# Optimization experiments

Hardware: AMD Instinct MI355X
Metric: run time of the kernel (lower is better)

## Reference

```python
import jax, jax.numpy as jnp
import numpy as np
from jax.scipy.linalg import expm

N, D, COND_DIM = 1152, 64, 1152
B, T = 16, 1024


def setup_inputs() -> dict:
    key = jax.random.key(0)
    k1, k2, k3, k4, k5 = jax.random.split(key, 5)
    x = jax.random.normal(k1, (B, T, N), dtype=jnp.float32)
    cond = jax.random.normal(k2, (B, COND_DIM), dtype=jnp.float32)
    # learned parameters
    P = jax.random.normal(k3, (N, D), dtype=jnp.float32)
    n_skew = D * (D - 1) // 2
    # nn.Linear default init: U(-1/sqrt(fan_in), 1/sqrt(fan_in))
    bound = 1.0 / np.sqrt(COND_DIM)
    W = jax.random.uniform(k4, (n_skew, COND_DIM), minval=-bound, maxval=bound, dtype=jnp.float32)
    b = jax.random.uniform(k5, (n_skew,), minval=-bound, maxval=bound, dtype=jnp.float32)
    return {"x": x, "cond": cond, "P": P, "W": W, "b": b}


def _rotation(cond, W, b):
    # SiLU -> Linear -> skew-symmetric A -> matrix exponential
    v = jax.nn.silu(cond) @ W.T + b  # (B, D*(D-1)//2)
    iu, ju = jnp.triu_indices(D, k=1)
    A = jnp.zeros((cond.shape[0], D, D), dtype=v.dtype)
    A = A.at[:, iu, ju].set(v).at[:, ju, iu].set(-v)
    return expm(A)  # batched over leading dim, (B, D, D)


def reference(x, cond, P, W, b):
    U, _ = jnp.linalg.qr(P)          # (N, D) orthonormal basis of subspace
    R = _rotation(cond, W, b)        # (B, D, D)
    z = jnp.einsum('btn,nd->btd', x, U)          # project into subspace
    z_rot = jnp.einsum('btd,bde->bte', z, R)     # rotate within subspace
    x_rot = x + jnp.einsum('btd,nd->btn', z_rot - z, U)  # (z_rot - z) @ U.T
    return x_rot
```

## Files before the change

kernel.cpp:

```cpp
#include <hip/hip_runtime.h>
#include <math.h>

#define NN 1152
#define DD 64
#define NSK 2016
#define NB 16
#define NROWS (NB*1024)
#define GPARTS 6

typedef short bf16x8 __attribute__((ext_vector_type(8)));
typedef float f32x4  __attribute__((ext_vector_type(4)));

__device__ __forceinline__ short bfr(float f){
  unsigned u = __float_as_uint(f);
  u += 0x7fffu + ((u >> 16) & 1u);
  return (short)(u >> 16);
}

__global__ __launch_bounds__(256) void k_pre(const float* __restrict__ cond, const float* __restrict__ W,
                                             const float* __restrict__ bias, float* __restrict__ v,
                                             const float* __restrict__ P, float* __restrict__ Gpart){
  __shared__ float Ps[64*68];
  __shared__ float red[256*17];
  const int tid = threadIdx.x;
  if (blockIdx.x < NSK){
    const int q = blockIdx.x;
    float acc[NB];
    #pragma unroll
    for (int b = 0; b < NB; ++b) acc[b] = 0.f;
    for (int c = tid; c < NN; c += 256){
      const float wv = W[q*NN + c];
      #pragma unroll
      for (int b = 0; b < NB; ++b){
        const float xv = cond[b*NN + c];
        const float s = xv / (1.f + __expf(-xv));
        acc[b] = fmaf(wv, s, acc[b]);
      }
    }
    #pragma unroll
    for (int b = 0; b < NB; ++b) red[tid*17 + b] = acc[b];
    __syncthreads();
    for (int off = 128; off > 0; off >>= 1){
      if (tid < off){
        #pragma unroll
        for (int b = 0; b < NB; ++b) red[tid*17 + b] += red[(tid+off)*17 + b];
      }
      __syncthreads();
    }
    if (tid < NB) v[tid*NSK + q] = red[tid] + bias[q];
  } else {
    const int p = blockIdx.x - NSK;
    const int lr = tid >> 4, lc = (tid & 15) * 4;
    const int ti = tid >> 4, tj = tid & 15;
    float acc[4][4];
    #pragma unroll
    for (int i=0;i<4;++i){
      #pragma unroll
      for (int j=0;j<4;++j) acc[i][j]=0.f;
    }
    for (int ch = 0; ch < 3; ++ch){
      const int n0 = p*192 + ch*64;
      __syncthreads();
      #pragma unroll
      for (int ii = 0; ii < 4; ++ii){
        const float4 pv = *(const float4*)&P[(n0 + lr + 16*ii)*DD + lc];
        *(float4*)&Ps[(lr + 16*ii)*68 + lc] = pv;
      }
      __syncthreads();
      for (int r = 0; r < 64; ++r){
        const float4 a = *(const float4*)&Ps[r*68 + ti*4];
        const float4 b = *(const float4*)&Ps[r*68 + tj*4];
        const float av[4] = {a.x,a.y,a.z,a.w};
        const float bv[4] = {b.x,b.y,b.z,b.w};
        #pragma unroll
        for (int i=0;i<4;++i){
          #pragma unroll
          for (int j=0;j<4;++j) acc[i][j] = fmaf(av[i], bv[j], acc[i][j]);
        }
      }
    }
    float* g = &Gpart[p*DD*DD];
    #pragma unroll
    for (int i=0;i<4;++i){
      float4 ov = make_float4(acc[i][0], acc[i][1], acc[i][2], acc[i][3]);
      *(float4*)&g[(ti*4+i)*DD + tj*4] = ov;
    }
  }
}

__device__ void qr_wave(const float* __restrict__ Gpart, const float* __restrict__ P,
                        float* __restrict__ Rout){
  const int j = threadIdx.x;
  float Gc[DD], Wc[DD], Rc[DD];
  #pragma unroll
  for (int i = 0; i < DD; ++i){
    float g = 0.f;
    #pragma unroll
    for (int p = 0; p < GPARTS; ++p) g += Gpart[p*4096 + i*DD + j];
    Gc[i] = g;
    Wc[i] = P[i*DD + j];
  }
  #pragma unroll
  for (int k = 0; k < DD; ++k){
    const float gkk = __shfl(Gc[k], k);
    const float wkk = __shfl(Wc[k], k);
    const float beta = (wkk >= 0.f) ? -sqrtf(gkk) : sqrtf(gkk);
    const float wkj = Wc[k];
    const float dj  = Gc[k] - beta*wkj;
    const float cj  = dj / (beta*(beta - wkk));
    float rkj = wkj + dj/beta;
    if (j == k) rkj = beta;
    if (j <  k) rkj = 0.f;
    Rc[k] = rkj;
    #pragma unroll
    for (int i = k+1; i < DD; ++i){
      const float wik = __shfl(Wc[i], k);
      const float rki = __shfl(rkj, i);
      Wc[i] = fmaf(-cj,  wik, Wc[i]);
      Gc[i] = fmaf(-rki, rkj, Gc[i]);
    }
  }
  #pragma unroll
  for (int i = 0; i < DD; ++i) Rout[i*DD + j] = Rc[i];
}

__device__ __forceinline__ void mmul68(const float* __restrict__ A, const float* __restrict__ B,
                                       float* __restrict__ C, int tid){
  __syncthreads();
  const int ty = tid >> 4, tx = tid & 15;
  float acc[4][4];
  #pragma unroll
  for (int i=0;i<4;++i){
    #pragma unroll
    for (int j=0;j<4;++j) acc[i][j]=0.f;
  }
  for (int kq = 0; kq < 16; ++kq){
    float4 a[4], b[4];
    #pragma unroll
    for (int i=0;i<4;++i) a[i] = *(const float4*)&A[(ty*4+i)*68 + kq*4];
    #pragma unroll
    for (int kk=0;kk<4;++kk) b[kk] = *(const float4*)&B[(kq*4+kk)*68 + tx*4];
    #pragma unroll
    for (int i=0;i<4;++i){
      const float av[4] = {a[i].x, a[i].y, a[i].z, a[i].w};
      #pragma unroll
      for (int kk=0;kk<4;++kk){
        acc[i][0] = fmaf(av[kk], b[kk].x, acc[i][0]);
        acc[i][1] = fmaf(av[kk], b[kk].y, acc[i][1]);
        acc[i][2] = fmaf(av[kk], b[kk].z, acc[i][2]);
        acc[i][3] = fmaf(av[kk], b[kk].w, acc[i][3]);
      }
    }
  }
  #pragma unroll
  for (int i=0;i<4;++i)
    *(float4*)&C[(ty*4+i)*68 + tx*4] = make_float4(acc[i][0],acc[i][1],acc[i][2],acc[i][3]);
  __syncthreads();
}

__global__ __launch_bounds__(256,1) void k_setup(const float* __restrict__ Gpart, const float* __restrict__ P,
                                                 float* __restrict__ Rout,
                                                 const float* __restrict__ v, float* __restrict__ Mg){
  __shared__ float Bs[64*68], B2[64*68], B3[64*68], Tb[64*68], Xb[64*68];
  __shared__ float ncol[DD];
  __shared__ float scl_s;
  __shared__ int   ssh_s;
  const int tid = threadIdx.x;
  if (blockIdx.x == NB){
    if (tid >= 64) return;
    qr_wave(Gpart, P, Rout);
    return;
  }
  const int b = blockIdx.x;
  for (int idx = tid; idx < 64*64; idx += 256)
    Xb[(idx>>6)*68 + (idx&63)] = 0.f;
  __syncthreads();
  for (int idx = tid; idx < NSK; idx += 256){
    int i = (int)((127.0f - sqrtf(16129.0f - 8.0f*(float)idx)) * 0.5f);
    while (i*(127 - i)/2 > idx) --i;
    while ((i+1)*(127 - (i+1))/2 <= idx) ++i;
    const int jj = idx - i*(127 - i)/2 + i + 1;
    const float val = v[b*NSK + idx];
    Xb[i*68 + jj] = val;
    Xb[jj*68 + i] = -val;
  }
  __syncthreads();
  if (tid < DD){
    float s = 0.f;
    for (int r = 0; r < DD; ++r) s += fabsf(Xb[r*68 + tid]);
    ncol[tid] = s;
  }
  __syncthreads();
  if (tid == 0){
    float nrm = 0.f;
    for (int c = 0; c < DD; ++c) nrm = fmaxf(nrm, ncol[c]);
    int s = 0; float scale = 1.f;
    while (nrm > 1.0f && s < 40){ nrm *= 0.5f; scale *= 0.5f; ++s; }
    ssh_s = s; scl_s = scale;
  }
  __syncthreads();
  const float scale = scl_s;
  const int   sq    = ssh_s;
  for (int idx = tid; idx < 64*64; idx += 256){
    const int i = idx>>6, jj = idx&63;
    Bs[i*68 + jj] = Xb[i*68 + jj] * scale;
  }
  mmul68(Bs, Bs, B2, tid);
  mmul68(B2, Bs, B3, tid);
  for (int idx = tid; idx < 64*64; idx += 256){
    const int i = idx>>6, jj = idx&63;
    const int o = i*68 + jj;
    Tb[o] = (i==jj ? (1.f/720.f) : 0.f) + Bs[o]*(1.f/5040.f) + B2[o]*(1.f/40320.f) + B3[o]*(1.f/362880.f);
  }
  mmul68(B3, Tb, Xb, tid);
  for (int idx = tid; idx < 64*64; idx += 256){
    const int i = idx>>6, jj = idx&63;
    const int o = i*68 + jj;
    Xb[o] += (i==jj ? (1.f/6.f) : 0.f) + Bs[o]*(1.f/24.f) + B2[o]*(1.f/120.f);
  }
  mmul68(B3, Xb, Tb, tid);
  for (int idx = tid; idx < 64*64; idx += 256){
    const int i = idx>>6, jj = idx&63;
    const int o = i*68 + jj;
    Tb[o] += (i==jj ? 1.f : 0.f) + Bs[o] + B2[o]*0.5f;
  }
  float* cur = Tb;
  float* oth = Xb;
  for (int r = 0; r < sq; ++r){
    mmul68(cur, cur, oth, tid);
    float* t = cur; cur = oth; oth = t;
  }
  for (int idx = tid; idx < 64*64; idx += 256){
    const int i = idx>>6, jj = idx&63;
    Mg[b*4096 + idx] = cur[i*68 + jj] - (i==jj ? 1.f : 0.f);
  }
}

__global__ __launch_bounds__(64) void k_solveU(const float* __restrict__ P, const float* __restrict__ Rg,
                                               short* __restrict__ Ubf, short* __restrict__ Utbf){
  __shared__ float Rs[DD*DD];
  __shared__ float Ps[DD*65];
  __shared__ float rd[DD];
  const int tid = threadIdx.x;
  const int n0 = blockIdx.x * DD;
  for (int r = 0; r < DD; ++r){
    Rs[r*DD + tid] = Rg[r*DD + tid];
    Ps[r*65 + tid] = P[(n0 + r)*DD + tid];
  }
  rd[tid] = 1.f / Rg[tid*DD + tid];
  __syncthreads();
  float u[DD];
  #pragma unroll
  for (int j = 0; j < DD; ++j){
    float s0 = Ps[tid*65 + j], s1 = 0.f;
    #pragma unroll
    for (int l = 0; l + 1 < j; l += 2){
      s0 = fmaf(-u[l],   Rs[l*DD + j],     s0);
      s1 = fmaf(-u[l+1], Rs[(l+1)*DD + j], s1);
    }
    if (j & 1) s0 = fmaf(-u[j-1], Rs[(j-1)*DD + j], s0);
    u[j] = (s0 + s1) * rd[j];
  }
  #pragma unroll
  for (int d = 0; d < DD; ++d)
    Utbf[d*NN + n0 + tid] = bfr(u[d]);
  #pragma unroll
  for (int j8 = 0; j8 < 8; ++j8){
    bf16x8 pk;
    #pragma unroll
    for (int jj = 0; jj < 8; ++jj) pk[jj] = bfr(u[j8*8 + jj]);
    *(bf16x8*)&Ubf[(n0 + tid)*DD + j8*8] = pk;
  }
}

__global__ __launch_bounds__(512,1) void k_main(const float* __restrict__ x, const short* __restrict__ Ubf,
                                                const short* __restrict__ Utbf, const float* __restrict__ Mg,
                                                float* __restrict__ out){
  __shared__ float zs[64*68];
  __shared__ float Ms[64*68];
  __shared__ short wbf[64*72];
  const int tid  = threadIdx.x;
  const int lane = tid & 63, wid = tid >> 6;
  const int row0 = blockIdx.x * 64;
  const int bb   = row0 >> 10;
  const int m    = lane & 15, quad = lane >> 4;
  for (int idx = tid; idx < 64*64; idx += 512)
    Ms[(idx>>6)*68 + (idx&63)] = Mg[bb*4096 + idx];

  const int r0 = (wid & 3) * 16;
  const int c0 = (wid >> 2) * 32;
  f32x4 acc0 = {0.f,0.f,0.f,0.f}, acc1 = {0.f,0.f,0.f,0.f};
  const float* xrow = &x[(row0 + r0 + m)*NN + quad*8];
  const short* ut0  = &Utbf[(c0      + m)*NN + quad*8];
  const short* ut1  = &Utbf[(c0 + 16 + m)*NN + quad*8];
  float4 xa = *(const float4*)(xrow);
  float4 xb = *(const float4*)(xrow + 4);
  bf16x8 b0 = *(const bf16x8*)(ut0);
  bf16x8 b1 = *(const bf16x8*)(ut1);
  for (int kc = 0; kc < NN; kc += 32){
    float4 nxa, nxb; bf16x8 nb0, nb1;
    if (kc + 32 < NN){
      nxa = *(const float4*)(xrow + kc + 32);
      nxb = *(const float4*)(xrow + kc + 36);
      nb0 = *(const bf16x8*)(ut0 + kc + 32);
      nb1 = *(const bf16x8*)(ut1 + kc + 32);
    }
    bf16x8 a;
    a[0]=bfr(xa.x); a[1]=bfr(xa.y); a[2]=bfr(xa.z); a[3]=bfr(xa.w);
    a[4]=bfr(xb.x); a[5]=bfr(xb.y); a[6]=bfr(xb.z); a[7]=bfr(xb.w);
    acc0 = __builtin_amdgcn_mfma_f32_16x16x32_bf16(a, b0, acc0, 0, 0, 0);
    acc1 = __builtin_amdgcn_mfma_f32_16x16x32_bf16(a, b1, acc1, 0, 0, 0);
    xa = nxa; xb = nxb; b0 = nb0; b1 = nb1;
  }
  #pragma unroll
  for (int q = 0; q < 4; ++q){
    zs[(r0 + quad*4 + q)*68 + c0      + m] = acc0[q];
    zs[(r0 + quad*4 + q)*68 + c0 + 16 + m] = acc1[q];
  }
  __syncthreads();

  {
    const int r  = tid >> 3;
    const int cc = (tid & 7) * 8;
    float w0[8];
    #pragma unroll
    for (int jj = 0; jj < 8; ++jj) w0[jj] = 0.f;
    for (int k = 0; k < 64; ++k){
      const float zr = zs[r*68 + k];
      const float4 m0 = *(const float4*)&Ms[k*68 + cc];
      const float4 m1 = *(const float4*)&Ms[k*68 + cc + 4];
      w0[0] = fmaf(zr, m0.x, w0[0]); w0[1] = fmaf(zr, m0.y, w0[1]);
      w0[2] = fmaf(zr, m0.z, w0[2]); w0[3] = fmaf(zr, m0.w, w0[3]);
      w0[4] = fmaf(zr, m1.x, w0[4]); w0[5] = fmaf(zr, m1.y, w0[5]);
      w0[6] = fmaf(zr, m1.z, w0[6]); w0[7] = fmaf(zr, m1.w, w0[7]);
    }
    bf16x8 pk;
    #pragma unroll
    for (int jj = 0; jj < 8; ++jj) pk[jj] = bfr(w0[jj]);
    *(bf16x8*)&wbf[r*72 + cc] = pk;
  }
  __syncthreads();

  bf16x8 wa0 = *(const bf16x8*)&wbf[(r0 + m)*72 +      quad*8];
  bf16x8 wa1 = *(const bf16x8*)&wbf[(r0 + m)*72 + 32 + quad*8];
  const int colpar = wid >> 2;
  for (int it = 0; it < 36; ++it){
    const int n0 = (colpar + 2*it) * 16;
    bf16x8 ub0 = *(const bf16x8*)&Ubf[(n0 + m)*DD +      quad*8];
    bf16x8 ub1 = *(const bf16x8*)&Ubf[(n0 + m)*DD + 32 + quad*8];
    f32x4 acc = {0.f,0.f,0.f,0.f};
    acc = __builtin_amdgcn_mfma_f32_16x16x32_bf16(wa0, ub0, acc, 0, 0, 0);
    acc = __builtin_amdgcn_mfma_f32_16x16x32_bf16(wa1, ub1, acc, 0, 0, 0);
    #pragma unroll
    for (int q = 0; q < 4; ++q){
      const int r = row0 + r0 + quad*4 + q;
      const int c = n0 + m;
      out[r*NN + c] = x[r*NN + c] + acc[q];
    }
  }
}

extern "C" void kernel_launch(void* const* d_in, const int* in_sizes, int n_in,
                              void* d_out, int out_size, void* d_ws, size_t ws_size,
                              hipStream_t stream) {
  const float* x    = (const float*)d_in[0];
  const float* cond = (const float*)d_in[1];
  const float* P    = (const float*)d_in[2];
  const float* W    = (const float*)d_in[3];
  const float* bias = (const float*)d_in[4];
  float* out = (float*)d_out;
  float* ws  = (float*)d_ws;

  float* Gpart = ws;
  float* Rbuf  = ws + 24576;
  float* vbuf  = ws + 28672;
  float* Mg    = ws + 61440;
  short* Ubf   = (short*)(ws + 126976);
  short* Utbf  = (short*)(ws + 163840);

  hipLaunchKernelGGL(k_pre,   dim3(NSK + GPARTS), dim3(256), 0, stream, cond, W, bias, vbuf, P, Gpart);
  hipLaunchKernelGGL(k_setup, dim3(NB + 1),       dim3(256), 0, stream, Gpart, P, Rbuf, vbuf, Mg);
  hipLaunchKernelGGL(k_solveU,dim3(NN/DD),        dim3(64),  0, stream, P, Rbuf, Ubf, Utbf);
  hipLaunchKernelGGL(k_main,  dim3(NROWS/64),     dim3(512), 0, stream, x, Ubf, Utbf, Mg, out);
}
```

Before: 285.2 us.

## Shrink main-kernel row tiles for occupancy and restructure conditioning GEMV

The main kernel now handles 16 rows per 256-thread block instead of 64 rows per 512-thread block, with launch bounds allowing 4 blocks per CU, and double-buffers x/U loads with a 64-wide k step. Its output phase prefetches the next U tile. The SiLU+linear prologue now computes SiLU once per block into shared memory, assigns one wave per output row using float4 loads, and reduces with wave shuffles instead of a shared-memory tree. The aim is more latency hiding and less redundant SiLU work, at the cost of loading the 64x64 M matrix four times as often and reading each U tile from more blocks.

Result: slower. 319.5 us (+12.0%).

```diff
diff --git a/kernel.cpp b/kernel.cpp
--- a/kernel.cpp
+++ b/kernel.cpp
@@ -7,8 +7,11 @@
 #define NB 16
 #define NROWS (NB*1024)
 #define GPARTS 6
+#define QPB 4
+#define VPB (NSK/QPB)
 
 typedef short bf16x8 __attribute__((ext_vector_type(8)));
+typedef short bf16x4 __attribute__((ext_vector_type(4)));
 typedef float f32x4  __attribute__((ext_vector_type(4)));
 
 __device__ __forceinline__ short bfr(float f){
@@ -20,36 +23,49 @@
 __global__ __launch_bounds__(256) void k_pre(const float* __restrict__ cond, const float* __restrict__ W,
                                              const float* __restrict__ bias, float* __restrict__ v,
                                              const float* __restrict__ P, float* __restrict__ Gpart){
-  __shared__ float Ps[64*68];
-  __shared__ float red[256*17];
+  __shared__ float smem[16*1160];
   const int tid = threadIdx.x;
-  if (blockIdx.x < NSK){
-    const int q = blockIdx.x;
+  if (blockIdx.x < VPB){
+    #pragma unroll
+    for (int b = 0; b < NB; ++b){
+      for (int c = tid; c < NN; c += 256){
+        const float xv = cond[b*NN + c];
+        smem[b*1160 + c] = xv / (1.f + __expf(-xv));
+      }
+    }
+    __syncthreads();
+    const int lane = tid & 63, wid = tid >> 6;
+    const int q = blockIdx.x * QPB + wid;
     float acc[NB];
     #pragma unroll
     for (int b = 0; b < NB; ++b) acc[b] = 0.f;
-    for (int c = tid; c < NN; c += 256){
-      const float wv = W[q*NN + c];
+    for (int c0 = 0; c0 < NN; c0 += 256){
+      const int c = c0 + lane*4;
+      if (c < NN){
+        const float4 wv = *(const float4*)&W[q*NN + c];
+        #pragma unroll
+        for (int b = 0; b < NB; ++b){
+          const float4 sv = *(const float4*)&smem[b*1160 + c];
+          acc[b] = fmaf(wv.x, sv.x, acc[b]);
+          acc[b] = fmaf(wv.y, sv.y, acc[b]);
+          acc[b] = fmaf(wv.z, sv.z, acc[b]);
+          acc[b] = fmaf(wv.w, sv.w, acc[b]);
+        }
+      }
+    }
+    #pragma unroll
+    for (int off = 32; off > 0; off >>= 1){
       #pragma unroll
-      for (int b = 0; b < NB; ++b){
-        const float xv = cond[b*NN + c];
-        const float s = xv / (1.f + __expf(-xv));
-        acc[b] = fmaf(wv, s, acc[b]);
-      }
-    }
-    #pragma unroll
-    for (int b = 0; b < NB; ++b) red[tid*17 + b] = acc[b];
-    __syncthreads();
-    for (int off = 128; off > 0; off >>= 1){
-      if (tid < off){
-        #pragma unroll
-        for (int b = 0; b < NB; ++b) red[tid*17 + b] += red[(tid+off)*17 + b];
-      }
-      __syncthreads();
-    }
-    if (tid < NB) v[tid*NSK + q] = red[tid] + bias[q];
+      for (int b = 0; b < NB; ++b) acc[b] += __shfl_xor(acc[b], off);
+    }
+    if (lane == 0){
+      const float bq = bias[q];
+      #pragma unroll
+      for (int b = 0; b < NB; ++b) v[b*NSK + q] = acc[b] + bq;
+    }
   } else {
-    const int p = blockIdx.x - NSK;
+    float* Ps = smem;
+    const int p = blockIdx.x - VPB;
     const int lr = tid >> 4, lc = (tid & 15) * 4;
     const int ti = tid >> 4, tj = tid & 15;
     float acc[4][4];
@@ -273,91 +289,102 @@
   }
 }
 
-__global__ __launch_bounds__(512,1) void k_main(const float* __restrict__ x, const short* __restrict__ Ubf,
+#define PH1_STEP(XA,XB,UU) do { \
+    bf16x8 a_; \
+    a_[0]=bfr(XA.x); a_[1]=bfr(XA.y); a_[2]=bfr(XA.z); a_[3]=bfr(XA.w); \
+    a_[4]=bfr(XB.x); a_[5]=bfr(XB.y); a_[6]=bfr(XB.z); a_[7]=bfr(XB.w); \
+    acc0 = __builtin_amdgcn_mfma_f32_16x16x32_bf16(a_, UU, acc0, 0, 0, 0); \
+  } while(0)
+
+#define PH3_BODY(NC) do { \
+    const float xq0 = x[(row0 + quad*4 + 0)*NN + (NC) + m]; \
+    const float xq1 = x[(row0 + quad*4 + 1)*NN + (NC) + m]; \
+    const float xq2 = x[(row0 + quad*4 + 2)*NN + (NC) + m]; \
+    const float xq3 = x[(row0 + quad*4 + 3)*NN + (NC) + m]; \
+    f32x4 acc = {0.f,0.f,0.f,0.f}; \
+    acc = __builtin_amdgcn_mfma_f32_16x16x32_bf16(wa0, ub0, acc, 0, 0, 0); \
+    acc = __builtin_amdgcn_mfma_f32_16x16x32_bf16(wa1, ub1, acc, 0, 0, 0); \
+    out[(row0 + quad*4 + 0)*NN + (NC) + m] = xq0 + acc[0]; \
+    out[(row0 + quad*4 + 1)*NN + (NC) + m] = xq1 + acc[1]; \
+    out[(row0 + quad*4 + 2)*NN + (NC) + m] = xq2 + acc[2]; \
+    out[(row0 + quad*4 + 3)*NN + (NC) + m] = xq3 + acc[3]; \
+  } while(0)
+
+__global__ __launch_bounds__(256,4) void k_main(const float* __restrict__ x, const short* __restrict__ Ubf,
                                                 const short* __restrict__ Utbf, const float* __restrict__ Mg,
                                                 float* __restrict__ out){
-  __shared__ float zs[64*68];
   __shared__ float Ms[64*68];
-  __shared__ short wbf[64*72];
+  __shared__ float zs[16*68];
+  __shared__ short wbf[16*72];
   const int tid  = threadIdx.x;
   const int lane = tid & 63, wid = tid >> 6;
-  const int row0 = blockIdx.x * 64;
+  const int row0 = blockIdx.x * 16;
   const int bb   = row0 >> 10;
   const int m    = lane & 15, quad = lane >> 4;
-  for (int idx = tid; idx < 64*64; idx += 512)
+  for (int idx = tid; idx < 64*64; idx += 256)
     Ms[(idx>>6)*68 + (idx&63)] = Mg[bb*4096 + idx];
 
-  const int r0 = (wid & 3) * 16;
-  const int c0 = (wid >> 2) * 32;
-  f32x4 acc0 = {0.f,0.f,0.f,0.f}, acc1 = {0.f,0.f,0.f,0.f};
-  const float* xrow = &x[(row0 + r0 + m)*NN + quad*8];
-  const short* ut0  = &Utbf[(c0      + m)*NN + quad*8];
-  const short* ut1  = &Utbf[(c0 + 16 + m)*NN + quad*8];
-  float4 xa = *(const float4*)(xrow);
-  float4 xb = *(const float4*)(xrow + 4);
-  bf16x8 b0 = *(const bf16x8*)(ut0);
-  bf16x8 b1 = *(const bf16x8*)(ut1);
-  for (int kc = 0; kc < NN; kc += 32){
-    float4 nxa, nxb; bf16x8 nb0, nb1;
-    if (kc + 32 < NN){
-      nxa = *(const float4*)(xrow + kc + 32);
-      nxb = *(const float4*)(xrow + kc + 36);
-      nb0 = *(const bf16x8*)(ut0 + kc + 32);
-      nb1 = *(const bf16x8*)(ut1 + kc + 32);
-    }
-    bf16x8 a;
-    a[0]=bfr(xa.x); a[1]=bfr(xa.y); a[2]=bfr(xa.z); a[3]=bfr(xa.w);
-    a[4]=bfr(xb.x); a[5]=bfr(xb.y); a[6]=bfr(xb.z); a[7]=bfr(xb.w);
-    acc0 = __builtin_amdgcn_mfma_f32_16x16x32_bf16(a, b0, acc0, 0, 0, 0);
-    acc1 = __builtin_amdgcn_mfma_f32_16x16x32_bf16(a, b1, acc1, 0, 0, 0);
-    xa = nxa; xb = nxb; b0 = nb0; b1 = nb1;
-  }
-  #pragma unroll
-  for (int q = 0; q < 4; ++q){
-    zs[(r0 + quad*4 + q)*68 + c0      + m] = acc0[q];
-    zs[(r0 + quad*4 + q)*68 + c0 + 16 + m] = acc1[q];
-  }
+  const int c0 = wid * 16;
+  const float* xrow = &x[(row0 + m)*NN + quad*8];
+  const short* utp  = &Utbf[(c0 + m)*NN + quad*8];
+  f32x4 acc0 = {0.f,0.f,0.f,0.f};
+  float4 xa0 = *(const float4*)(xrow);
+  float4 xb0 = *(const float4*)(xrow + 4);
+  float4 xa1 = *(const float4*)(xrow + 32);
+  float4 xb1 = *(const float4*)(xrow + 36);
+  bf16x8 u0  = *(const bf16x8*)(utp);
+  bf16x8 u1  = *(const bf16x8*)(utp + 32);
+  for (int kc = 0; kc < NN - 64; kc += 64){
+    const float4 pxa0 = *(const float4*)(xrow + kc + 64);
+    const float4 pxb0 = *(const float4*)(xrow + kc + 68);
+    const bf16x8 pu0  = *(const bf16x8*)(utp + kc + 64);
+    const float4 pxa1 = *(const float4*)(xrow + kc + 96);
+    const float4 pxb1 = *(const float4*)(xrow + kc + 100);
+    const bf16x8 pu1  = *(const bf16x8*)(utp + kc + 96);
+    PH1_STEP(xa0, xb0, u0);
+    PH1_STEP(xa1, xb1, u1);
+    xa0 = pxa0; xb0 = pxb0; u0 = pu0;
+    xa1 = pxa1; xb1 = pxb1; u1 = pu1;
+  }
+  PH1_STEP(xa0, xb0, u0);
+  PH1_STEP(xa1, xb1, u1);
+  #pragma unroll
+  for (int q = 0; q < 4; ++q)
+    zs[(quad*4 + q)*68 + c0 + m] = acc0[q];
   __syncthreads();
 
   {
-    const int r  = tid >> 3;
-    const int cc = (tid & 7) * 8;
-    float w0[8];
-    #pragma unroll
-    for (int jj = 0; jj < 8; ++jj) w0[jj] = 0.f;
+    const int r  = tid >> 4;
+    const int cc = (tid & 15) * 4;
+    float w0[4] = {0.f,0.f,0.f,0.f};
     for (int k = 0; k < 64; ++k){
       const float zr = zs[r*68 + k];
       const float4 m0 = *(const float4*)&Ms[k*68 + cc];
-      const float4 m1 = *(const float4*)&Ms[k*68 + cc + 4];
-      w0[0] = fmaf(zr, m0.x, w0[0]); w0[1] = fmaf(zr, m0.y, w0[1]);
-      w0[2] = fmaf(zr, m0.z, w0[2]); w0[3] = fmaf(zr, m0.w, w0[3]);
-      w0[4] = fmaf(zr, m1.x, w0[4]); w0[5] = fmaf(zr, m1.y, w0[5]);
-      w0[6] = fmaf(zr, m1.z, w0[6]); w0[7] = fmaf(zr, m1.w, w0[7]);
-    }
-    bf16x8 pk;
-    #pragma unroll
-    for (int jj = 0; jj < 8; ++jj) pk[jj] = bfr(w0[jj]);
-    *(bf16x8*)&wbf[r*72 + cc] = pk;
-  }
-  __syncthreads();
-
-  bf16x8 wa0 = *(const bf16x8*)&wbf[(r0 + m)*72 +      quad*8];
-  bf16x8 wa1 = *(const bf16x8*)&wbf[(r0 + m)*72 + 32 + quad*8];
-  const int colpar = wid >> 2;
-  for (int it = 0; it < 36; ++it){
-    const int n0 = (colpar + 2*it) * 16;
-    bf16x8 ub0 = *(const bf16x8*)&Ubf[(n0 + m)*DD +      quad*8];
-    bf16x8 ub1 = *(const bf16x8*)&Ubf[(n0 + m)*DD + 32 + quad*8];
-    f32x4 acc = {0.f,0.f,0.f,0.f};
-    acc = __builtin_amdgcn_mfma_f32_16x16x32_bf16(wa0, ub0, acc, 0, 0, 0);
-    acc = __builtin_amdgcn_mfma_f32_16x16x32_bf16(wa1, ub1, acc, 0, 0, 0);
-    #pragma unroll
-    for (int q = 0; q < 4; ++q){
-      const int r = row0 + r0 + quad*4 + q;
-      const int c = n0 + m;
-      out[r*NN + c] = x[r*NN + c] + acc[q];
-    }
-  }
+      w0[0] = fmaf(zr, m0.x, w0[0]);
+      w0[1] = fmaf(zr, m0.y, w0[1]);
+      w0[2] = fmaf(zr, m0.z, w0[2]);
+      w0[3] = fmaf(zr, m0.w, w0[3]);
+    }
+    bf16x4 pk;
+    #pragma unroll
+    for (int jj = 0; jj < 4; ++jj) pk[jj] = bfr(w0[jj]);
+    *(bf16x4*)&wbf[r*72 + cc] = pk;
+  }
+  __syncthreads();
+
+  bf16x8 wa0 = *(const bf16x8*)&wbf[m*72 +      quad*8];
+  bf16x8 wa1 = *(const bf16x8*)&wbf[m*72 + 32 + quad*8];
+  bf16x8 ub0 = *(const bf16x8*)&Ubf[(wid*16 + m)*DD +      quad*8];
+  bf16x8 ub1 = *(const bf16x8*)&Ubf[(wid*16 + m)*DD + 32 + quad*8];
+  for (int it = 0; it < 17; ++it){
+    const int n0c = (wid + 4*it) * 16;
+    const int n1  = n0c + 64;
+    const bf16x8 nb0 = *(const bf16x8*)&Ubf[(n1 + m)*DD +      quad*8];
+    const bf16x8 nb1 = *(const bf16x8*)&Ubf[(n1 + m)*DD + 32 + quad*8];
+    PH3_BODY(n0c);
+    ub0 = nb0; ub1 = nb1;
+  }
+  PH3_BODY((wid + 68) * 16);
 }
 
 extern "C" void kernel_launch(void* const* d_in, const int* in_sizes, int n_in,
@@ -378,8 +405,8 @@
   short* Ubf   = (short*)(ws + 126976);
   short* Utbf  = (short*)(ws + 163840);
 
-  hipLaunchKernelGGL(k_pre,   dim3(NSK + GPARTS), dim3(256), 0, stream, cond, W, bias, vbuf, P, Gpart);
+  hipLaunchKernelGGL(k_pre,   dim3(VPB + GPARTS), dim3(256), 0, stream, cond, W, bias, vbuf, P, Gpart);
   hipLaunchKernelGGL(k_setup, dim3(NB + 1),       dim3(256), 0, stream, Gpart, P, Rbuf, vbuf, Mg);
   hipLaunchKernelGGL(k_solveU,dim3(NN/DD),        dim3(64),  0, stream, P, Rbuf, Ubf, Utbf);
-  hipLaunchKernelGGL(k_main,  dim3(NROWS/64),     dim3(512), 0, stream, x, Ubf, Utbf, Mg, out);
-}
+  hipLaunchKernelGGL(k_main,  dim3(NROWS/16),     dim3(256), 0, stream, x, Ubf, Utbf, Mg, out);
+}
```

## Use MFMA split-K for cond linear and split main kernel into zw and output passes

Applied to the files above, without the earlier changes.

The SiLU-linear producing the skew parameters now runs as bf16 MFMA tiles split over six K partitions. The partial sums are reduced, with the bias added, inside the setup kernel. This replaces the per-output-row block with its shared-memory tree reduction. The main kernel is also split in two: one computes the rotated projection w and writes it to global memory as bf16, and a new lighter output kernel with many more blocks does the U^T expansion plus residual with prefetched loads. The split is meant to raise occupancy and parallelism for the store-bound phase, at the cost of an extra kernel launch, a second read of x, and bf16 rounding of cond and W.

After: 265.7 us. -6.8%, faster.

```diff
diff --git a/kernel.cpp b/kernel.cpp
--- a/kernel.cpp
+++ b/kernel.cpp
@@ -7,8 +7,12 @@
 #define NB 16
 #define NROWS (NB*1024)
 #define GPARTS 6
+#define KPARTS 6
+#define VNBLK 32
+#define VBLKS (VNBLK*KPARTS)
 
 typedef short bf16x8 __attribute__((ext_vector_type(8)));
+typedef short bf16x4 __attribute__((ext_vector_type(4)));
 typedef float f32x4  __attribute__((ext_vector_type(4)));
 
 __device__ __forceinline__ short bfr(float f){
@@ -18,38 +22,42 @@
 }
 
 __global__ __launch_bounds__(256) void k_pre(const float* __restrict__ cond, const float* __restrict__ W,
-                                             const float* __restrict__ bias, float* __restrict__ v,
+                                             float* __restrict__ vpart,
                                              const float* __restrict__ P, float* __restrict__ Gpart){
   __shared__ float Ps[64*68];
-  __shared__ float red[256*17];
   const int tid = threadIdx.x;
-  if (blockIdx.x < NSK){
-    const int q = blockIdx.x;
-    float acc[NB];
-    #pragma unroll
-    for (int b = 0; b < NB; ++b) acc[b] = 0.f;
-    for (int c = tid; c < NN; c += 256){
-      const float wv = W[q*NN + c];
+  if (blockIdx.x < VBLKS){
+    const int nb = blockIdx.x / KPARTS;
+    const int kp = blockIdx.x % KPARTS;
+    const int lane = tid & 63, wid = tid >> 6;
+    const int m = lane & 15, quad = lane >> 4;
+    const int n0 = nb*64 + wid*16;
+    if (n0 >= NSK) return;
+    f32x4 acc = {0.f,0.f,0.f,0.f};
+    const float* crow = &cond[m*NN + kp*192 + quad*8];
+    const float* wrow = &W[(n0 + m)*NN + kp*192 + quad*8];
+    #pragma unroll
+    for (int c = 0; c < 6; ++c){
+      const float4 ca = *(const float4*)(crow + c*32);
+      const float4 cb = *(const float4*)(crow + c*32 + 4);
+      const float4 wa = *(const float4*)(wrow + c*32);
+      const float4 wb = *(const float4*)(wrow + c*32 + 4);
+      bf16x8 a, b;
+      const float cv[8] = {ca.x,ca.y,ca.z,ca.w,cb.x,cb.y,cb.z,cb.w};
+      const float wv[8] = {wa.x,wa.y,wa.z,wa.w,wb.x,wb.y,wb.z,wb.w};
       #pragma unroll
-      for (int b = 0; b < NB; ++b){
-        const float xv = cond[b*NN + c];
-        const float s = xv / (1.f + __expf(-xv));
-        acc[b] = fmaf(wv, s, acc[b]);
+      for (int j = 0; j < 8; ++j){
+        const float xv = cv[j];
+        a[j] = bfr(xv / (1.f + __expf(-xv)));
+        b[j] = bfr(wv[j]);
       }
-    }
-    #pragma unroll
-    for (int b = 0; b < NB; ++b) red[tid*17 + b] = acc[b];
-    __syncthreads();
-    for (int off = 128; off > 0; off >>= 1){
-      if (tid < off){
-        #pragma unroll
-        for (int b = 0; b < NB; ++b) red[tid*17 + b] += red[(tid+off)*17 + b];
-      }
-      __syncthreads();
-    }
-    if (tid < NB) v[tid*NSK + q] = red[tid] + bias[q];
+      acc = __builtin_amdgcn_mfma_f32_16x16x32_bf16(a, b, acc, 0, 0, 0);
+    }
+    #pragma unroll
+    for (int r = 0; r < 4; ++r)
+      vpart[(kp*16 + quad*4 + r)*NSK + n0 + m] = acc[r];
   } else {
-    const int p = blockIdx.x - NSK;
+    const int p = blockIdx.x - VBLKS;
     const int lr = tid >> 4, lc = (tid & 15) * 4;
     const int ti = tid >> 4, tj = tid & 15;
     float acc[4][4];
@@ -59,11 +67,11 @@
       for (int j=0;j<4;++j) acc[i][j]=0.f;
     }
     for (int ch = 0; ch < 3; ++ch){
-      const int n0 = p*192 + ch*64;
+      const int nn0 = p*192 + ch*64;
       __syncthreads();
       #pragma unroll
       for (int ii = 0; ii < 4; ++ii){
-        const float4 pv = *(const float4*)&P[(n0 + lr + 16*ii)*DD + lc];
+        const float4 pv = *(const float4*)&P[(nn0 + lr + 16*ii)*DD + lc];
         *(float4*)&Ps[(lr + 16*ii)*68 + lc] = pv;
       }
       __syncthreads();
@@ -160,7 +168,8 @@
 
 __global__ __launch_bounds__(256,1) void k_setup(const float* __restrict__ Gpart, const float* __restrict__ P,
                                                  float* __restrict__ Rout,
-                                                 const float* __restrict__ v, float* __restrict__ Mg){
+                                                 const float* __restrict__ vpart, const float* __restrict__ bias,
+                                                 float* __restrict__ Mg){
   __shared__ float Bs[64*68], B2[64*68], B3[64*68], Tb[64*68], Xb[64*68];
   __shared__ float ncol[DD];
   __shared__ float scl_s;
@@ -180,7 +189,9 @@
     while (i*(127 - i)/2 > idx) --i;
     while ((i+1)*(127 - (i+1))/2 <= idx) ++i;
     const int jj = idx - i*(127 - i)/2 + i + 1;
-    const float val = v[b*NSK + idx];
+    float val = bias[idx];
+    #pragma unroll
+    for (int p = 0; p < KPARTS; ++p) val += vpart[(p*16 + b)*NSK + idx];
     Xb[i*68 + jj] = val;
     Xb[jj*68 + i] = -val;
   }
@@ -273,12 +284,10 @@
   }
 }
 
-__global__ __launch_bounds__(512,1) void k_main(const float* __restrict__ x, const short* __restrict__ Ubf,
-                                                const short* __restrict__ Utbf, const float* __restrict__ Mg,
-                                                float* __restrict__ out){
+__global__ __launch_bounds__(512,1) void k_zw(const float* __restrict__ x, const short* __restrict__ Utbf,
+                                              const float* __restrict__ Mg, short* __restrict__ wg){
   __shared__ float zs[64*68];
   __shared__ float Ms[64*68];
-  __shared__ short wbf[64*72];
   const int tid  = threadIdx.x;
   const int lane = tid & 63, wid = tid >> 6;
   const int row0 = blockIdx.x * 64;
@@ -319,44 +328,63 @@
   }
   __syncthreads();
 
-  {
-    const int r  = tid >> 3;
-    const int cc = (tid & 7) * 8;
-    float w0[8];
-    #pragma unroll
-    for (int jj = 0; jj < 8; ++jj) w0[jj] = 0.f;
-    for (int k = 0; k < 64; ++k){
-      const float zr = zs[r*68 + k];
-      const float4 m0 = *(const float4*)&Ms[k*68 + cc];
-      const float4 m1 = *(const float4*)&Ms[k*68 + cc + 4];
-      w0[0] = fmaf(zr, m0.x, w0[0]); w0[1] = fmaf(zr, m0.y, w0[1]);
-      w0[2] = fmaf(zr, m0.z, w0[2]); w0[3] = fmaf(zr, m0.w, w0[3]);
-      w0[4] = fmaf(zr, m1.x, w0[4]); w0[5] = fmaf(zr, m1.y, w0[5]);
-      w0[6] = fmaf(zr, m1.z, w0[6]); w0[7] = fmaf(zr, m1.w, w0[7]);
-    }
-    bf16x8 pk;
-    #pragma unroll
-    for (int jj = 0; jj < 8; ++jj) pk[jj] = bfr(w0[jj]);
-    *(bf16x8*)&wbf[r*72 + cc] = pk;
-  }
-  __syncthreads();
-
-  bf16x8 wa0 = *(const bf16x8*)&wbf[(r0 + m)*72 +      quad*8];
-  bf16x8 wa1 = *(const bf16x8*)&wbf[(r0 + m)*72 + 32 + quad*8];
-  const int colpar = wid >> 2;
-  for (int it = 0; it < 36; ++it){
-    const int n0 = (colpar + 2*it) * 16;
-    bf16x8 ub0 = *(const bf16x8*)&Ubf[(n0 + m)*DD +      quad*8];
-    bf16x8 ub1 = *(const bf16x8*)&Ubf[(n0 + m)*DD + 32 + quad*8];
+  const int r  = tid >> 3;
+  const int cc = (tid & 7) * 8;
+  float w0[8];
+  #pragma unroll
+  for (int jj = 0; jj < 8; ++jj) w0[jj] = 0.f;
+  for (int k = 0; k < 64; ++k){
+    const float zr = zs[r*68 + k];
+    const float4 m0 = *(const float4*)&Ms[k*68 + cc];
+    const float4 m1 = *(const float4*)&Ms[k*68 + cc + 4];
+    w0[0] = fmaf(zr, m0.x, w0[0]); w0[1] = fmaf(zr, m0.y, w0[1]);
+    w0[2] = fmaf(zr, m0.z, w0[2]); w0[3] = fmaf(zr, m0.w, w0[3]);
+    w0[4] = fmaf(zr, m1.x, w0[4]); w0[5] = fmaf(zr, m1.y, w0[5]);
+    w0[6] = fmaf(zr, m1.z, w0[6]); w0[7] = fmaf(zr, m1.w, w0[7]);
+  }
+  bf16x8 pk;
+  #pragma unroll
+  for (int jj = 0; jj < 8; ++jj) pk[jj] = bfr(w0[jj]);
+  *(bf16x8*)&wg[(row0 + r)*DD + cc] = pk;
+}
+
+__global__ __launch_bounds__(256) void k_out(const float* __restrict__ x, const short* __restrict__ Ubf,
+                                             const short* __restrict__ wg, float* __restrict__ out){
+  const int tid  = threadIdx.x;
+  const int lane = tid & 63, wid = tid >> 6;
+  const int row0 = blockIdx.x * 16;
+  const int m    = lane & 15, quad = lane >> 4;
+  const int q4   = quad * 4;
+  bf16x8 wa0 = *(const bf16x8*)&wg[(row0 + m)*DD +      quad*8];
+  bf16x8 wa1 = *(const bf16x8*)&wg[(row0 + m)*DD + 32 + quad*8];
+  bf16x8 ub0 = *(const bf16x8*)&Ubf[(wid*16 + m)*DD +      quad*8];
+  bf16x8 ub1 = *(const bf16x8*)&Ubf[(wid*16 + m)*DD + 32 + quad*8];
+  float xq0 = x[(row0 + q4 + 0)*NN + wid*16 + m];
+  float xq1 = x[(row0 + q4 + 1)*NN + wid*16 + m];
+  float xq2 = x[(row0 + q4 + 2)*NN + wid*16 + m];
+  float xq3 = x[(row0 + q4 + 3)*NN + wid*16 + m];
+  for (int it = 0; it < 18; ++it){
+    const int n0 = (wid + 4*it) * 16;
     f32x4 acc = {0.f,0.f,0.f,0.f};
     acc = __builtin_amdgcn_mfma_f32_16x16x32_bf16(wa0, ub0, acc, 0, 0, 0);
     acc = __builtin_amdgcn_mfma_f32_16x16x32_bf16(wa1, ub1, acc, 0, 0, 0);
-    #pragma unroll
-    for (int q = 0; q < 4; ++q){
-      const int r = row0 + r0 + quad*4 + q;
-      const int c = n0 + m;
-      out[r*NN + c] = x[r*NN + c] + acc[q];
-    }
+    const float o0 = xq0 + acc[0];
+    const float o1 = xq1 + acc[1];
+    const float o2 = xq2 + acc[2];
+    const float o3 = xq3 + acc[3];
+    if (it < 17){
+      const int n1 = n0 + 64;
+      ub0 = *(const bf16x8*)&Ubf[(n1 + m)*DD +      quad*8];
+      ub1 = *(const bf16x8*)&Ubf[(n1 + m)*DD + 32 + quad*8];
+      xq0 = x[(row0 + q4 + 0)*NN + n1 + m];
+      xq1 = x[(row0 + q4 + 1)*NN + n1 + m];
+      xq2 = x[(row0 + q4 + 2)*NN + n1 + m];
+      xq3 = x[(row0 + q4 + 3)*NN + n1 + m];
+    }
+    out[(row0 + q4 + 0)*NN + n0 + m] = o0;
+    out[(row0 + q4 + 1)*NN + n0 + m] = o1;
+    out[(row0 + q4 + 2)*NN + n0 + m] = o2;
+    out[(row0 + q4 + 3)*NN + n0 + m] = o3;
   }
 }
 
@@ -373,13 +401,15 @@
 
   float* Gpart = ws;
   float* Rbuf  = ws + 24576;
-  float* vbuf  = ws + 28672;
-  float* Mg    = ws + 61440;
-  short* Ubf   = (short*)(ws + 126976);
-  short* Utbf  = (short*)(ws + 163840);
-
-  hipLaunchKernelGGL(k_pre,   dim3(NSK + GPARTS), dim3(256), 0, stream, cond, W, bias, vbuf, P, Gpart);
-  hipLaunchKernelGGL(k_setup, dim3(NB + 1),       dim3(256), 0, stream, Gpart, P, Rbuf, vbuf, Mg);
-  hipLaunchKernelGGL(k_solveU,dim3(NN/DD),        dim3(64),  0, stream, P, Rbuf, Ubf, Utbf);
-  hipLaunchKernelGGL(k_main,  dim3(NROWS/64),     dim3(512), 0, stream, x, Ubf, Utbf, Mg, out);
-}
+  float* vpart = ws + 28672;
+  float* Mg    = ws + 222208;
+  short* Ubf   = (short*)(ws + 287744);
+  short* Utbf  = (short*)(ws + 324608);
+  short* wg    = (short*)(ws + 361472);
+
+  hipLaunchKernelGGL(k_pre,   dim3(VBLKS + GPARTS), dim3(256), 0, stream, cond, W, vpart, P, Gpart);
+  hipLaunchKernelGGL(k_setup, dim3(NB + 1),         dim3(256), 0, stream, Gpart, P, Rbuf, vpart, bias, Mg);
+  hipLaunchKernelGGL(k_solveU,dim3(NN/DD),          dim3(64),  0, stream, P, Rbuf, Ubf, Utbf);
+  hipLaunchKernelGGL(k_zw,    dim3(NROWS/64),       dim3(512), 0, stream, x, Utbf, Mg, wg);
+  hipLaunchKernelGGL(k_out,   dim3(NROWS/16),       dim3(256), 0, stream, x, Ubf, wg, out);
+}
```
